# Optimization experiments

Hardware: AMD Instinct MI355X
Metric: run time of the kernel (lower is better)

## Reference

```python
import jax, jax.numpy as jnp
import numpy as np

INPUT_SIZE = 20
HIDDEN = 51
OUT = 1
B = 4096
T = 512


def _init_lstm_params(key, in_dim, hid_dim):
    # PyTorch LSTMCell init: U(-1/sqrt(hid), 1/sqrt(hid))
    k = 1.0 / np.sqrt(hid_dim)
    ks = jax.random.split(key, 4)
    W_ih = jax.random.uniform(ks[0], (4 * hid_dim, in_dim), minval=-k, maxval=k, dtype=jnp.float32)
    W_hh = jax.random.uniform(ks[1], (4 * hid_dim, hid_dim), minval=-k, maxval=k, dtype=jnp.float32)
    b_ih = jax.random.uniform(ks[2], (4 * hid_dim,), minval=-k, maxval=k, dtype=jnp.float32)
    b_hh = jax.random.uniform(ks[3], (4 * hid_dim,), minval=-k, maxval=k, dtype=jnp.float32)
    return W_ih, W_hh, b_ih, b_hh


def setup_inputs() -> dict:
    key = jax.random.key(0)
    k_x, k1, k2, k3, k4 = jax.random.split(key, 5)
    x = jax.random.normal(k_x, (B, T, INPUT_SIZE), dtype=jnp.float32)
    W_ih1, W_hh1, b_ih1, b_hh1 = _init_lstm_params(k1, INPUT_SIZE, HIDDEN)
    W_ih2, W_hh2, b_ih2, b_hh2 = _init_lstm_params(k2, HIDDEN, OUT)
    kl = 1.0 / np.sqrt(OUT)
    ka, kb, kc, kd = jax.random.split(k3, 4)
    W_mu = jax.random.uniform(ka, (OUT, OUT), minval=-kl, maxval=kl, dtype=jnp.float32)
    b_mu = jax.random.uniform(kb, (OUT,), minval=-kl, maxval=kl, dtype=jnp.float32)
    W_lv = jax.random.uniform(kc, (OUT, OUT), minval=-kl, maxval=kl, dtype=jnp.float32)
    b_lv = jax.random.uniform(kd, (OUT,), minval=-kl, maxval=kl, dtype=jnp.float32)
    return {
        "x": x,
        "W_ih1": W_ih1, "W_hh1": W_hh1, "b_ih1": b_ih1, "b_hh1": b_hh1,
        "W_ih2": W_ih2, "W_hh2": W_hh2, "b_ih2": b_ih2, "b_hh2": b_hh2,
        "W_mu": W_mu, "b_mu": b_mu, "W_lv": W_lv, "b_lv": b_lv,
    }


def _lstm_cell(x_t, h, c, W_ih, W_hh, b_ih, b_hh):
    # PyTorch LSTMCell: gate order i, f, g, o
    gates = x_t @ W_ih.T + b_ih + h @ W_hh.T + b_hh
    i, f, g, o = jnp.split(gates, 4, axis=-1)
    c_new = jax.nn.sigmoid(f) * c + jax.nn.sigmoid(i) * jnp.tanh(g)
    h_new = jax.nn.sigmoid(o) * jnp.tanh(c_new)
    return h_new, c_new


def reference(x, W_ih1, W_hh1, b_ih1, b_hh1, W_ih2, W_hh2, b_ih2, b_hh2, W_mu, b_mu, W_lv, b_lv):
    bsz = x.shape[0]
    h1 = jnp.zeros((bsz, HIDDEN), dtype=x.dtype)
    c1 = jnp.zeros((bsz, HIDDEN), dtype=x.dtype)
    h2 = jnp.zeros((bsz, OUT), dtype=x.dtype)
    c2 = jnp.zeros((bsz, OUT), dtype=x.dtype)

    def step(carry, x_t):
        h1, c1, h2, c2 = carry
        h1, c1 = _lstm_cell(x_t, h1, c1, W_ih1, W_hh1, b_ih1, b_hh1)
        h2, c2 = _lstm_cell(h1, h2, c2, W_ih2, W_hh2, b_ih2, b_hh2)
        return (h1, c1, h2, c2), h2

    xs = jnp.swapaxes(x, 0, 1)  # [T, B, input_size]
    _, h2_seq = jax.lax.scan(step, (h1, c1, h2, c2), xs)  # h2_seq: [T, B, 1]
    agg = jnp.mean(h2_seq, axis=0)  # [B, 1] mean over time
    mu = agg @ W_mu.T + b_mu
    log_var = agg @ W_lv.T + b_lv
    sigma = jnp.exp(0.5 * log_var)
    lower = mu - 1.96 * sigma
    upper = mu + 1.96 * sigma
    return (lower, mu, upper, log_var)
```

## Files before the change

### kernel.cpp

```cpp
#include <hip/hip_runtime.h>

#define B_TOT 4096
#define T_STEPS 512
#define IN 20
#define HID 51

typedef float f32x4 __attribute__((ext_vector_type(4)));
typedef short s16x8 __attribute__((ext_vector_type(8)));

__device__ __forceinline__ unsigned short f2bf(float f) {
    unsigned int u = __float_as_uint(f);
    unsigned int r = (u + 0x7fffu + ((u >> 16) & 1u)) >> 16;
    return (unsigned short)r;
}

#define L2E  1.4426950408889634f
#define L2E2 2.8853900817779268f

__device__ __forceinline__ float fast_rcp(float x) { return __builtin_amdgcn_rcpf(x); }
__device__ __forceinline__ float ex2(float x)      { return __builtin_amdgcn_exp2f(x); }
__device__ __forceinline__ float sig_p(float p)  { return fast_rcp(1.0f + ex2(p)); }
__device__ __forceinline__ float tanh_q(float q) { return 1.0f - 2.0f * fast_rcp(1.0f + ex2(q)); }
__device__ __forceinline__ float tanh2_q(float q) {
    return __builtin_fmaf(fast_rcp(1.0f + ex2(q)), -2.0f * L2E2, L2E2);
}


__global__ __launch_bounds__(1024)
void lstm_fused(const float* __restrict__ x,
                const float* __restrict__ Wih1, const float* __restrict__ Whh1,
                const float* __restrict__ bih1, const float* __restrict__ bhh1,
                const float* __restrict__ Wih2, const float* __restrict__ Whh2,
                const float* __restrict__ bih2, const float* __restrict__ bhh2,
                const float* __restrict__ Wmu,  const float* __restrict__ bmu,
                const float* __restrict__ Wlv,  const float* __restrict__ blv,
                float* __restrict__ out)
{
    __shared__ __align__(16) unsigned short vA[2][2][64][8];
    __shared__ __align__(16) unsigned short xS[4][64][8];

    const int tid  = threadIdx.x;
    const int lane = tid & 63;
    const int w    = tid >> 6;
    const int bidx = blockIdx.x;

    const bool isT  = (w <= 12);
    const bool isST = (w == 13);
    const bool isL2 = (w == 14);

    s16x8 wfrag[3];
    f32x4 binit = {0.f, 0.f, 0.f, 0.f};
    {
        const int m = lane & 15;
        #pragma unroll
        for (int ks = 0; ks < 3; ++ks) {
            s16x8 f;
            #pragma unroll
            for (int j = 0; j < 8; ++j) {
                int k = ks * 32 + ((lane >> 4) << 3) + j;
                float v = 0.0f;
                if (isT) {
                    int g = m & 3, unit = w * 4 + (m >> 2);
                    if (unit < HID) {
                        int row = g * HID + unit;
                        if (k < IN) v = Wih1[row * IN + k];
                        else if (k >= 32 && k < 32 + HID) v = Whh1[row * HID + (k - 32)];
                        v *= (g == 2) ? L2E2 : -L2E;
                    }
                }
                f[j] = (short)f2bf(v);
            }
            wfrag[ks] = f;
        }
        if (isT) {
            int unit = w * 4 + (lane >> 4);
            if (unit < HID) {
                #pragma unroll
                for (int r = 0; r < 4; ++r)
                    binit[r] = (bih1[r * HID + unit] + bhh1[r * HID + unit]) * ((r == 2) ? L2E2 : -L2E);
            }
        }
    }

    int hchunk = 0, hrow = 0, hj = 0;
    if (isT) {
        int unit = w * 4 + (lane >> 4);
        int k    = 32 + unit;
        hchunk = (k >> 5) - 1;
        hrow   = (((k >> 3) & 3) << 4) + (lane & 15);
        hj     = k & 7;
    }

    s16x8 l2frag[2];
    f32x4 l2binit = {0.f, 0.f, 0.f, 0.f};
    float whh2g[4] = {0.f, 0.f, 0.f, 0.f};
    if (isL2) {
        const int m = lane & 15;
        #pragma unroll
        for (int ks = 1; ks < 3; ++ks) {
            s16x8 f;
            #pragma unroll
            for (int j = 0; j < 8; ++j) {
                int k = ks * 32 + ((lane >> 4) << 3) + j;
                float v = 0.0f;
                if (m < 4 && k >= 32 && k < 32 + HID)
                    v = Wih2[m * HID + (k - 32)] * ((m == 2) ? L2E2 : -L2E);
                f[j] = (short)f2bf(v);
            }
            l2frag[ks - 1] = f;
        }
        #pragma unroll
        for (int r = 0; r < 4; ++r) {
            float s = (r == 2) ? L2E2 : -L2E;
            whh2g[r]   = Whh2[r] * s;
            l2binit[r] = (bih2[r] + bhh2[r]) * s;
        }
    }

    const float* sp[5];
    int srow[5], sj[5];
    if (isST) {
        #pragma unroll
        for (int i = 0; i < 5; ++i) {
            int e = i * 64 + lane;
            int b = e / IN, m = e % IN;
            sp[i]   = x + ((size_t)(bidx * 16 + b) * T_STEPS) * IN + m;
            srow[i] = ((m >> 3) & 3) * 16 + b;
            sj[i]   = m & 7;
        }
    }

    {
        unsigned short* vz = &vA[0][0][0][0];
        for (int i = tid; i < 2 * 2 * 64 * 8; i += 1024) vz[i] = 0;
        unsigned short* xz = &xS[0][0][0];
        for (int i = tid; i < 4 * 64 * 8; i += 1024) xz[i] = 0;
    }
    __syncthreads();
    float rE[5], rO[5];
    if (isST) {
        #pragma unroll
        for (int i = 0; i < 5; ++i) {
            xS[0][srow[i]][sj[i]] = f2bf(sp[i][0]);
            xS[1][srow[i]][sj[i]] = f2bf(sp[i][IN]);
            rE[i] = sp[i][(size_t)2 * IN];
            rO[i] = sp[i][(size_t)3 * IN];
        }
    }
    __syncthreads();

    f32x4 accx = {0.f, 0.f, 0.f, 0.f};
    if (isT) {
        const s16x8 b00 = *(const s16x8*)&xS[0][lane][0];
        accx = __builtin_amdgcn_mfma_f32_16x16x32_bf16(wfrag[0], b00, binit, 0, 0, 0);
    }

    float C1t = 0.f;
    float C2p = 0.f, h2p = 0.f, sum2 = 0.f;

#define STEP(tt, P, XR, XW, XREG)                                                \
    {                                                                            \
        if (isST) {                                                              \
            const int t4 = ((tt) < T_STEPS - 4) ? (tt) + 4 : T_STEPS - 1;        \
            _Pragma("unroll")                                                    \
            for (int i = 0; i < 5; ++i) {                                        \
                xS[XW][srow[i]][sj[i]] = f2bf(XREG[i]);                          \
                XREG[i] = sp[i][(size_t)t4 * IN];                                \
            }                                                                    \
        }                                                                        \
        if (isT) {                                                               \
            const s16x8 bf1 = *(const s16x8*)&vA[P][0][lane][0];                 \
            const s16x8 bf2 = *(const s16x8*)&vA[P][1][lane][0];                 \
            f32x4 a = accx;                                                      \
            a = __builtin_amdgcn_mfma_f32_16x16x32_bf16(wfrag[1], bf1, a, 0, 0, 0); \
            a = __builtin_amdgcn_mfma_f32_16x16x32_bf16(wfrag[2], bf2, a, 0, 0, 0); \
            float C = sig_p(a[1]) * C1t + sig_p(a[0]) * tanh2_q(a[2]);           \
            C1t = C;                                                             \
            float h = sig_p(a[3]) * tanh_q(C);                                   \
            vA[(P) ^ 1][hchunk][hrow][hj] = f2bf(h);                             \
            const s16x8 bf0n = *(const s16x8*)&xS[XR][lane][0];                  \
            accx = __builtin_amdgcn_mfma_f32_16x16x32_bf16(wfrag[0], bf0n, binit, 0, 0, 0); \
        }                                                                        \
        if (isL2) {                                                              \
            const s16x8 bf1 = *(const s16x8*)&vA[P][0][lane][0];                 \
            const s16x8 bf2 = *(const s16x8*)&vA[P][1][lane][0];                 \
            f32x4 a = l2binit;                                                   \
            a = __builtin_amdgcn_mfma_f32_16x16x32_bf16(l2frag[0], bf1, a, 0, 0, 0); \
            a = __builtin_amdgcn_mfma_f32_16x16x32_bf16(l2frag[1], bf2, a, 0, 0, 0); \
            if ((tt) > 0 && lane < 16) {                                         \
                float pi = a[0] + whh2g[0] * h2p;                                \
                float pf = a[1] + whh2g[1] * h2p;                                \
                float pg = a[2] + whh2g[2] * h2p;                                \
                float po = a[3] + whh2g[3] * h2p;                                \
                float C2 = sig_p(pf) * C2p + sig_p(pi) * tanh2_q(pg);            \
                C2p = C2;                                                        \
                h2p = sig_p(po) * tanh_q(C2);                                    \
                sum2 += h2p;                                                     \
            }                                                                    \
        }                                                                        \
        __syncthreads();                                                         \
    }

    for (int t = 0; t < T_STEPS; t += 4) {
        STEP(t + 0, 0, 1, 2, rE)
        STEP(t + 1, 1, 2, 3, rO)
        STEP(t + 2, 0, 3, 0, rE)
        STEP(t + 3, 1, 0, 1, rO)
    }
#undef STEP

    if (isL2) {
        s16x8 bf1 = *(const s16x8*)&vA[0][0][lane][0];
        s16x8 bf2 = *(const s16x8*)&vA[0][1][lane][0];
        f32x4 a = l2binit;
        a = __builtin_amdgcn_mfma_f32_16x16x32_bf16(l2frag[0], bf1, a, 0, 0, 0);
        a = __builtin_amdgcn_mfma_f32_16x16x32_bf16(l2frag[1], bf2, a, 0, 0, 0);
        if (lane < 16) {
            float pi = a[0] + whh2g[0] * h2p;
            float pf = a[1] + whh2g[1] * h2p;
            float pg = a[2] + whh2g[2] * h2p;
            float po = a[3] + whh2g[3] * h2p;
            float C2 = sig_p(pf) * C2p + sig_p(pi) * tanh2_q(pg);
            h2p = sig_p(po) * tanh_q(C2);
            sum2 += h2p;

            float agg = sum2 * (1.0f / 512.0f);
            float mu  = Wmu[0] * agg + bmu[0];
            float lv  = Wlv[0] * agg + blv[0];
            float sg  = __expf(0.5f * lv);
            int bg = bidx * 16 + lane;
            out[bg]             = mu - 1.96f * sg;
            out[B_TOT + bg]     = mu;
            out[2 * B_TOT + bg] = mu + 1.96f * sg;
            out[3 * B_TOT + bg] = lv;
        }
    }
}

extern "C" void kernel_launch(void* const* d_in, const int* in_sizes, int n_in,
                              void* d_out, int out_size, void* d_ws, size_t ws_size,
                              hipStream_t stream) {
    const float* x    = (const float*)d_in[0];
    const float* Wih1 = (const float*)d_in[1];
    const float* Whh1 = (const float*)d_in[2];
    const float* bih1 = (const float*)d_in[3];
    const float* bhh1 = (const float*)d_in[4];
    const float* Wih2 = (const float*)d_in[5];
    const float* Whh2 = (const float*)d_in[6];
    const float* bih2 = (const float*)d_in[7];
    const float* bhh2 = (const float*)d_in[8];
    const float* Wmu  = (const float*)d_in[9];
    const float* bmu  = (const float*)d_in[10];
    const float* Wlv  = (const float*)d_in[11];
    const float* blv  = (const float*)d_in[12];
    float* out = (float*)d_out;

    lstm_fused<<<dim3(B_TOT / 16), dim3(1024), 0, stream>>>(
        x, Wih1, Whh1, bih1, bhh1, Wih2, Whh2, bih2, bhh2, Wmu, bmu, Wlv, blv, out);
}
```

Baseline: 428.5 us.

## Fold layer-2 LSTM into spare rows of last tile wave, drop extra waves

The dedicated layer-2 wave and the idle 16th wave are removed, so each block now runs 14 waves instead of 16. The layer-2 input-gate rows are packed into the unused M rows of the tile that covers hidden units 48-50, renumbered so that wave 2 holds it. Layer 2 is computed one step late from the saved accumulator. The layer-1 cell math is also rewritten with a single combined reciprocal over the gate exponentials, cutting the number of rcp ops per step. This is meant to shorten the per-step critical path and lower barrier cost, at the risk of putting more serial work on wave 2 and changing overflow behaviour in the combined-reciprocal form.

```diff
diff --git a/kernel.cpp b/kernel.cpp
--- a/kernel.cpp
+++ b/kernel.cpp
@@ -26,7 +26,7 @@
 }
 
 
-__global__ __launch_bounds__(1024)
+__global__ __launch_bounds__(896)
 void lstm_fused(const float* __restrict__ x,
                 const float* __restrict__ Wih1, const float* __restrict__ Whh1,
                 const float* __restrict__ bih1, const float* __restrict__ bhh1,
@@ -44,9 +44,10 @@
     const int w    = tid >> 6;
     const int bidx = blockIdx.x;
 
-    const bool isT  = (w <= 12);
-    const bool isST = (w == 13);
-    const bool isL2 = (w == 14);
+    const int  tile  = (w == 2) ? 12 : (w == 12) ? 2 : w;
+    const bool isT   = (w <= 12);
+    const bool isFAT = (w == 2);
+    const bool isST  = (w == 13);
 
     s16x8 wfrag[3];
     f32x4 binit = {0.f, 0.f, 0.f, 0.f};
@@ -60,12 +61,18 @@
                 int k = ks * 32 + ((lane >> 4) << 3) + j;
                 float v = 0.0f;
                 if (isT) {
-                    int g = m & 3, unit = w * 4 + (m >> 2);
-                    if (unit < HID) {
-                        int row = g * HID + unit;
-                        if (k < IN) v = Wih1[row * IN + k];
-                        else if (k >= 32 && k < 32 + HID) v = Whh1[row * HID + (k - 32)];
-                        v *= (g == 2) ? L2E2 : -L2E;
+                    if (isFAT && m >= 12) {
+                        int g2 = m - 12;
+                        if (k >= 32 && k < 32 + HID)
+                            v = Wih2[g2 * HID + (k - 32)] * ((g2 == 2) ? L2E2 : -L2E);
+                    } else {
+                        int g = m & 3, unit = tile * 4 + (m >> 2);
+                        if (unit < HID) {
+                            int row = g * HID + unit;
+                            if (k < IN) v = Wih1[row * IN + k];
+                            else if (k >= 32 && k < 32 + HID) v = Whh1[row * HID + (k - 32)];
+                            v *= (g == 2) ? L2E2 : -L2E;
+                        }
                     }
                 }
                 f[j] = (short)f2bf(v);
@@ -73,48 +80,34 @@
             wfrag[ks] = f;
         }
         if (isT) {
-            int unit = w * 4 + (lane >> 4);
-            if (unit < HID) {
+            if (isFAT && (lane >> 4) == 3) {
                 #pragma unroll
                 for (int r = 0; r < 4; ++r)
-                    binit[r] = (bih1[r * HID + unit] + bhh1[r * HID + unit]) * ((r == 2) ? L2E2 : -L2E);
+                    binit[r] = (bih2[r] + bhh2[r]) * ((r == 2) ? L2E2 : -L2E);
+            } else {
+                int unit = tile * 4 + (lane >> 4);
+                if (unit < HID) {
+                    #pragma unroll
+                    for (int r = 0; r < 4; ++r)
+                        binit[r] = (bih1[r * HID + unit] + bhh1[r * HID + unit]) * ((r == 2) ? L2E2 : -L2E);
+                }
             }
         }
+    }
+
+    float whh2g[4] = {0.f, 0.f, 0.f, 0.f};
+    if (isFAT) {
+        #pragma unroll
+        for (int r = 0; r < 4; ++r) whh2g[r] = Whh2[r] * ((r == 2) ? L2E2 : -L2E);
     }
 
     int hchunk = 0, hrow = 0, hj = 0;
     if (isT) {
-        int unit = w * 4 + (lane >> 4);
+        int unit = tile * 4 + (lane >> 4);
         int k    = 32 + unit;
         hchunk = (k >> 5) - 1;
         hrow   = (((k >> 3) & 3) << 4) + (lane & 15);
         hj     = k & 7;
-    }
-
-    s16x8 l2frag[2];
-    f32x4 l2binit = {0.f, 0.f, 0.f, 0.f};
-    float whh2g[4] = {0.f, 0.f, 0.f, 0.f};
-    if (isL2) {
-        const int m = lane & 15;
-        #pragma unroll
-        for (int ks = 1; ks < 3; ++ks) {
-            s16x8 f;
-            #pragma unroll
-            for (int j = 0; j < 8; ++j) {
-                int k = ks * 32 + ((lane >> 4) << 3) + j;
-                float v = 0.0f;
-                if (m < 4 && k >= 32 && k < 32 + HID)
-                    v = Wih2[m * HID + (k - 32)] * ((m == 2) ? L2E2 : -L2E);
-                f[j] = (short)f2bf(v);
-            }
-            l2frag[ks - 1] = f;
-        }
-        #pragma unroll
-        for (int r = 0; r < 4; ++r) {
-            float s = (r == 2) ? L2E2 : -L2E;
-            whh2g[r]   = Whh2[r] * s;
-            l2binit[r] = (bih2[r] + bhh2[r]) * s;
-        }
     }
 
     const float* sp[5];
@@ -132,9 +125,9 @@
 
     {
         unsigned short* vz = &vA[0][0][0][0];
-        for (int i = tid; i < 2 * 2 * 64 * 8; i += 1024) vz[i] = 0;
+        for (int i = tid; i < 2 * 2 * 64 * 8; i += 896) vz[i] = 0;
         unsigned short* xz = &xS[0][0][0];
-        for (int i = tid; i < 4 * 64 * 8; i += 1024) xz[i] = 0;
+        for (int i = tid; i < 4 * 64 * 8; i += 896) xz[i] = 0;
     }
     __syncthreads();
     float rE[5], rO[5];
@@ -157,6 +150,7 @@
 
     float C1t = 0.f;
     float C2p = 0.f, h2p = 0.f, sum2 = 0.f;
+    f32x4 aP = {0.f, 0.f, 0.f, 0.f};
 
 #define STEP(tt, P, XR, XW, XREG)                                                \
     {                                                                            \
@@ -169,34 +163,36 @@
             }                                                                    \
         }                                                                        \
         if (isT) {                                                               \
-            const s16x8 bf1 = *(const s16x8*)&vA[P][0][lane][0];                 \
-            const s16x8 bf2 = *(const s16x8*)&vA[P][1][lane][0];                 \
-            f32x4 a = accx;                                                      \
-            a = __builtin_amdgcn_mfma_f32_16x16x32_bf16(wfrag[1], bf1, a, 0, 0, 0); \
-            a = __builtin_amdgcn_mfma_f32_16x16x32_bf16(wfrag[2], bf2, a, 0, 0, 0); \
-            float C = sig_p(a[1]) * C1t + sig_p(a[0]) * tanh2_q(a[2]);           \
-            C1t = C;                                                             \
-            float h = sig_p(a[3]) * tanh_q(C);                                   \
-            vA[(P) ^ 1][hchunk][hrow][hj] = f2bf(h);                             \
+            const s16x8 bf1  = *(const s16x8*)&vA[P][0][lane][0];                \
+            const s16x8 bf2  = *(const s16x8*)&vA[P][1][lane][0];                \
             const s16x8 bf0n = *(const s16x8*)&xS[XR][lane][0];                  \
-            accx = __builtin_amdgcn_mfma_f32_16x16x32_bf16(wfrag[0], bf0n, binit, 0, 0, 0); \
-        }                                                                        \
-        if (isL2) {                                                              \
-            const s16x8 bf1 = *(const s16x8*)&vA[P][0][lane][0];                 \
-            const s16x8 bf2 = *(const s16x8*)&vA[P][1][lane][0];                 \
-            f32x4 a = l2binit;                                                   \
-            a = __builtin_amdgcn_mfma_f32_16x16x32_bf16(l2frag[0], bf1, a, 0, 0, 0); \
-            a = __builtin_amdgcn_mfma_f32_16x16x32_bf16(l2frag[1], bf2, a, 0, 0, 0); \
-            if ((tt) > 0 && lane < 16) {                                         \
-                float pi = a[0] + whh2g[0] * h2p;                                \
-                float pf = a[1] + whh2g[1] * h2p;                                \
-                float pg = a[2] + whh2g[2] * h2p;                                \
-                float po = a[3] + whh2g[3] * h2p;                                \
+              \
+            if (isFAT && (tt) >= 2 && lane >= 48) {                              \
+                float pi = aP[0] + whh2g[0] * h2p;                               \
+                float pf = aP[1] + whh2g[1] * h2p;                               \
+                float pg = aP[2] + whh2g[2] * h2p;                               \
+                float po = aP[3] + whh2g[3] * h2p;                               \
                 float C2 = sig_p(pf) * C2p + sig_p(pi) * tanh2_q(pg);            \
                 C2p = C2;                                                        \
                 h2p = sig_p(po) * tanh_q(C2);                                    \
                 sum2 += h2p;                                                     \
             }                                                                    \
+            f32x4 a = accx;                                                      \
+            a = __builtin_amdgcn_mfma_f32_16x16x32_bf16(wfrag[1], bf1, a, 0, 0, 0); \
+            a = __builtin_amdgcn_mfma_f32_16x16x32_bf16(wfrag[2], bf2, a, 0, 0, 0); \
+            if (isFAT) aP = a;                                                   \
+                                        \
+            float ei = ex2(a[0]), ef = ex2(a[1]), eg = ex2(a[2]), eo = ex2(a[3]);\
+            float Pi = 1.f + ei, Pf = 1.f + ef, Pg = 1.f + eg, Po = 1.f + eo;    \
+            float Pig = Pi * Pg;                                                 \
+            float rr  = fast_rcp(Pf * Pig);                                      \
+            float C   = __builtin_fmaf(C1t, Pig, L2E2 * ((eg - 1.f) * Pf)) * rr; \
+            C1t = C;                                                             \
+            float ec  = ex2(fminf(C, 126.f));                                    \
+            float h   = (ec - 1.f) * fast_rcp(Po * (1.f + ec));                  \
+            if (!(isFAT && (lane >> 4) == 3))                                    \
+                vA[(P) ^ 1][hchunk][hrow][hj] = f2bf(h);                         \
+            accx = __builtin_amdgcn_mfma_f32_16x16x32_bf16(wfrag[0], bf0n, binit, 0, 0, 0); \
         }                                                                        \
         __syncthreads();                                                         \
     }
@@ -209,13 +205,23 @@
     }
 #undef STEP
 
-    if (isL2) {
-        s16x8 bf1 = *(const s16x8*)&vA[0][0][lane][0];
-        s16x8 bf2 = *(const s16x8*)&vA[0][1][lane][0];
-        f32x4 a = l2binit;
-        a = __builtin_amdgcn_mfma_f32_16x16x32_bf16(l2frag[0], bf1, a, 0, 0, 0);
-        a = __builtin_amdgcn_mfma_f32_16x16x32_bf16(l2frag[1], bf2, a, 0, 0, 0);
-        if (lane < 16) {
+    if (isFAT) {
+        if (lane >= 48) {
+            float pi = aP[0] + whh2g[0] * h2p;
+            float pf = aP[1] + whh2g[1] * h2p;
+            float pg = aP[2] + whh2g[2] * h2p;
+            float po = aP[3] + whh2g[3] * h2p;
+            float C2 = sig_p(pf) * C2p + sig_p(pi) * tanh2_q(pg);
+            C2p = C2;
+            h2p = sig_p(po) * tanh_q(C2);
+            sum2 += h2p;
+        }
+        const s16x8 bf1 = *(const s16x8*)&vA[0][0][lane][0];
+        const s16x8 bf2 = *(const s16x8*)&vA[0][1][lane][0];
+        f32x4 a = accx;
+        a = __builtin_amdgcn_mfma_f32_16x16x32_bf16(wfrag[1], bf1, a, 0, 0, 0);
+        a = __builtin_amdgcn_mfma_f32_16x16x32_bf16(wfrag[2], bf2, a, 0, 0, 0);
+        if (lane >= 48) {
             float pi = a[0] + whh2g[0] * h2p;
             float pf = a[1] + whh2g[1] * h2p;
             float pg = a[2] + whh2g[2] * h2p;
@@ -228,7 +234,7 @@
             float mu  = Wmu[0] * agg + bmu[0];
             float lv  = Wlv[0] * agg + blv[0];
             float sg  = __expf(0.5f * lv);
-            int bg = bidx * 16 + lane;
+            int bg = bidx * 16 + (lane & 15);
             out[bg]             = mu - 1.96f * sg;
             out[B_TOT + bg]     = mu;
             out[2 * B_TOT + bg] = mu + 1.96f * sg;
@@ -255,6 +261,6 @@
     const float* blv  = (const float*)d_in[12];
     float* out = (float*)d_out;
 
-    lstm_fused<<<dim3(B_TOT / 16), dim3(1024), 0, stream>>>(
+    lstm_fused<<<dim3(B_TOT / 16), dim3(896), 0, stream>>>(
         x, Wih1, Whh1, bih1, bhh1, Wih2, Whh2, bih2, bhh2, Wmu, bmu, Wlv, blv, out);
 }
```

Measured after the change: 431.2 us. Within noise of the previous version (+0.6%).
